# Kernel optimization log

Measured on AMD Instinct MI355X. Metric: run time of the kernel, lower is better.

## Reference

```python
import jax, jax.numpy as jnp
import numpy as np

EPS = 1e-4          # self.epsilon
STENCIL = 24        # fixed neighbor count


def _apply_G(x, coeffs, neighbors, N):
    """SpMV: y_i = G_ii * x_i + sum_j G_ij * x_{nbr[i,j]}.
    x: [B,N,1], coeffs: [B,N,25], neighbors: [B,N,24] (>=N means invalid)."""
    B = x.shape[0]
    mask = neighbors < N                                   # [B,N,24]
    safe = jnp.where(mask, neighbors, 0)
    x2 = x[..., 0]                                         # [B,N]
    x_nbrs = jnp.take_along_axis(x2, safe.reshape(B, -1), axis=1)
    x_nbrs = x_nbrs.reshape(B, -1, STENCIL) * mask.astype(x.dtype)
    res = x2 * coeffs[:, :, 0] + (x_nbrs * coeffs[:, :, 1:]).sum(axis=2)
    return res[..., None]                                  # [B,N,1]


def _apply_GT(x, coeffs, neighbors, N):
    """Transpose SpMV (scatter-add): y_{nbr[i,j]} += G_ij * x_i."""
    B = x.shape[0]
    mask = neighbors < N
    tgt = jnp.where(mask, neighbors, 0)                    # safe targets; masked vals are 0
    vals = (x * coeffs[:, :, 1:]) * mask.astype(x.dtype)   # [B,N,24]
    res = x[..., 0] * coeffs[:, :, 0]                      # [B,N]
    res = jax.vmap(lambda r, t, v: r.at[t].add(v))(
        res, tgt.reshape(B, -1), vals.reshape(B, -1))
    return res[..., None]                                  # [B,N,1]


def setup_inputs() -> dict:
    key = jax.random.key(0)
    kG, kAd, kAo, kw, kn = jax.random.split(key, 5)
    B, N = 2, 262144
    G_coeffs = jax.random.normal(kG, (B, N, 25), dtype=jnp.float32)
    A_diag = jax.random.normal(kAd, (B, N, 1), dtype=jnp.float32)
    A_off = jax.random.normal(kAo, (B, N, STENCIL), dtype=jnp.float32)
    w = jax.random.normal(kw, (B, N, 1), dtype=jnp.float32)
    valid_mask = jnp.ones((B, N, 1), dtype=jnp.float32)
    neighbors = jax.random.randint(kn, (B, N, STENCIL), 0, 270000, dtype=jnp.int64)
    return {"G_coeffs": G_coeffs, "A_diag": A_diag, "A_off": A_off,
            "w": w, "valid_mask": valid_mask, "neighbors": neighbors}


def reference(G_coeffs, A_diag, A_off, w, valid_mask, neighbors):
    B, N, _ = G_coeffs.shape
    active = valid_mask.sum()
    norm_A = (jnp.abs(A_diag).sum() + jnp.abs(A_off).sum()) / (active * 25 + 1e-6)
    # single probe vector (num_probe_vectors = 1)
    wm = w * valid_mask                                    # probe, masked
    u = _apply_GT(wm, G_coeffs, neighbors, N)
    v = _apply_G(u, G_coeffs, neighbors, N) + EPS * wm
    A_coeffs = jnp.concatenate([A_diag, A_off], axis=2)    # [B,N,25]
    y = _apply_G(v, A_coeffs, neighbors, N)
    z = y / (norm_A + 1e-8)
    diff = (z - wm) * valid_mask
    return (diff ** 2).sum() / (valid_mask.sum() + 1e-6)
```

## Files before the change

kernel.cpp:

```cpp
#include <hip/hip_runtime.h>
#include <stdint.h>

#define STENCIL 24
#define EPS_F 1e-4f
#define BLK 256
#define NXCD 8

#define NODE_N 262144
#define BIN_NODES 2048
#define LBINS 128
#define NBINS 256
#define BIN_CAP_G 49152

#define S_THREADS 512
#define S_EPT 16
#define EDGES_PER_BLOCK (S_THREADS * S_EPT)

typedef int   i32x2 __attribute__((ext_vector_type(2)));

template <typename T>
static __device__ __forceinline__ T ntload(const T* p) {
    return __builtin_nontemporal_load(p);
}

static __device__ __forceinline__ int get_xcc_id() {
    int x;
    asm volatile("s_getreg_b32 %0, hwreg(HW_REG_XCC_ID)" : "=s"(x));
    return x & (NXCD - 1);
}

__device__ __forceinline__ float wave_reduce_f32(float v) {
    #pragma unroll
    for (int off = 32; off > 0; off >>= 1)
        v += __shfl_down(v, off, 64);
    return v;
}

__device__ __forceinline__ float block_reduce_f32(float v) {
    __shared__ float sw[BLK / 64];
    float s = wave_reduce_f32(v);
    if ((threadIdx.x & 63) == 0) sw[threadIdx.x >> 6] = s;
    __syncthreads();
    float r = 0.f;
    if (threadIdx.x == 0) {
        #pragma unroll
        for (int k = 0; k < BLK / 64; ++k) r += sw[k];
    }
    return r;
}

__global__ void k_reduce(const float* __restrict__ Ad, const float* __restrict__ Ao,
                         const float* __restrict__ mask, long long BN,
                         float* __restrict__ pn, float* __restrict__ pa) {
    long long total = BN * STENCIL;
    long long stride = (long long)gridDim.x * blockDim.x;
    float s = 0.f, act = 0.f;
    for (long long t = (long long)blockIdx.x * blockDim.x + threadIdx.x; t < total; t += stride) {
        s += fabsf(ntload(Ao + t));
        if (t < BN) { s += fabsf(ntload(Ad + t)); act += ntload(mask + t); }
    }
    float bs = block_reduce_f32(s);
    if (threadIdx.x == 0) pn[blockIdx.x] = bs;
    __syncthreads();
    float ba = block_reduce_f32(act);
    if (threadIdx.x == 0) pa[blockIdx.x] = ba;
}

__global__ void k_scal(const float* __restrict__ pn, const float* __restrict__ pa,
                       int nblk, double* __restrict__ scal) {
    float sn = 0.f, sa = 0.f;
    for (int t = threadIdx.x; t < nblk; t += blockDim.x) { sn += pn[t]; sa += pa[t]; }
    float bn_ = block_reduce_f32(sn);
    __shared__ double dn;
    if (threadIdx.x == 0) dn = (double)bn_;
    __syncthreads();
    float ba = block_reduce_f32(sa);
    if (threadIdx.x == 0) {
        double act = (double)ba;
        scal[0] = dn / (act * 25.0 + 1e-6);
        scal[1] = act;
    }
}

__global__ __launch_bounds__(S_THREADS)
void k_sortscatter(const float* __restrict__ G, const float* __restrict__ w,
                   const float* __restrict__ mask, const int* __restrict__ nbr,
                   float* __restrict__ u, int* __restrict__ binCnt,
                   int2* __restrict__ pairs) {
    __shared__ int2 rec[EDGES_PER_BLOCK];
    __shared__ int hist[LBINS], incl[LBINS], excl[LBINS], pos[LBINS], gb[LBINS];
    int tid = threadIdx.x;
    if (tid < LBINS) hist[tid] = 0;
    __syncthreads();

    long long blockStart = (long long)blockIdx.x * EDGES_PER_BLOCK;
    long long t0 = blockStart + (long long)tid * S_EPT;

    int nb[S_EPT];
    const int4* p4 = (const int4*)(nbr + t0);
    #pragma unroll
    for (int q = 0; q < S_EPT / 4; ++q) {
        int4 x = p4[q];
        nb[q*4] = x.x; nb[q*4+1] = x.y; nb[q*4+2] = x.z; nb[q*4+3] = x.w;
    }
    #pragma unroll
    for (int e = 0; e < S_EPT; ++e) {
        unsigned n = (unsigned)nb[e];
        if (n < (unsigned)NODE_N) atomicAdd(&hist[n >> 11], 1);
    }
    __syncthreads();

    if (tid < LBINS) incl[tid] = hist[tid];
    __syncthreads();
    for (int d = 1; d < LBINS; d <<= 1) {
        int x = 0;
        if (tid < LBINS && tid >= d) x = incl[tid - d];
        __syncthreads();
        if (tid < LBINS) incl[tid] += x;
        __syncthreads();
    }
    int batchBase = (blockStart >= (long long)NODE_N * STENCIL) ? LBINS : 0;
    if (tid < LBINS) {
        int h = hist[tid];
        int ex = incl[tid] - h;
        excl[tid] = ex;
        pos[tid]  = ex;
        gb[tid]   = h ? atomicAdd(&binCnt[batchBase + tid], h) : 0;
    }
    __syncthreads();

    long long i0 = t0 / STENCIL;
    long long i1 = (t0 + S_EPT - 1) / STENCIL;
    float wm0 = w[i0] * mask[i0];
    float wm1 = (i1 != i0) ? w[i1] * mask[i1] : wm0;
    long long i = i0;
    int j = (int)(t0 - i0 * STENCIL);
    #pragma unroll
    for (int e = 0; e < S_EPT; ++e) {
        float wm = (i == i0) ? wm0 : wm1;
        if (j == 0) u[i] = wm * G[i * 25];
        unsigned n = (unsigned)nb[e];
        if (n < (unsigned)NODE_N) {
            int b = (int)(n >> 11);
            float val = wm * G[i * 25 + 1 + j];
            int lp = atomicAdd(&pos[b], 1);
            rec[lp] = make_int2((int)(n & (BIN_NODES - 1)) | (b << 11), __float_as_int(val));
        }
        if (++j == STENCIL) { j = 0; ++i; }
    }
    __syncthreads();

    int tot = incl[LBINS - 1];
    for (int s = tid; s < tot; s += S_THREADS) {
        int2 r = rec[s];
        int b = (r.x >> 11) & (LBINS - 1);
        int dst = gb[b] + (s - excl[b]);
        if (dst < BIN_CAP_G)
            pairs[(long long)(batchBase + b) * BIN_CAP_G + dst] =
                make_int2(r.x & (BIN_NODES - 1), r.y);
    }
}

__global__ __launch_bounds__(1024)
void k_binaccum(const int* __restrict__ binCnt, const int2* __restrict__ pairs,
                float* __restrict__ u) {
    __shared__ float acc[4][BIN_NODES + 1];
    int g = blockIdx.x, tid = threadIdx.x;
    for (int l = tid; l < BIN_NODES; l += 1024) {
        acc[0][l] = 0.f; acc[1][l] = 0.f; acc[2][l] = 0.f; acc[3][l] = 0.f;
    }
    __syncthreads();
    int cnt = binCnt[g]; if (cnt > BIN_CAP_G) cnt = BIN_CAP_G;
    const i32x2* pb = (const i32x2*)(pairs + (long long)g * BIN_CAP_G);
    int rep = tid & 3;
    for (int s = tid; s < cnt; s += 1024) {
        i32x2 r = __builtin_nontemporal_load(pb + s);
        atomicAdd(&acc[rep][r.x], __int_as_float(r.y));
    }
    __syncthreads();
    long long gbase = (long long)(g >> 7) * NODE_N + (long long)(g & (LBINS - 1)) * BIN_NODES;
    for (int l = tid; l < BIN_NODES; l += 1024)
        u[gbase + l] += acc[0][l] + acc[1][l] + acc[2][l] + acc[3][l];
}

__global__ __launch_bounds__(BLK)
void k_v(const float* __restrict__ G, const float* __restrict__ w,
         const float* __restrict__ mask, const int* __restrict__ nbr,
         const float* __restrict__ u, float* __restrict__ v, long long BN) {
    __shared__ float sg[BLK * 25];
    __shared__ int  snb[BLK * 25];
    int tid = threadIdx.x;
    long long base = (long long)blockIdx.x * BLK;
    int rows = (int)(((BN - base) < BLK) ? (BN - base) : BLK);
    const float* gsrc = G + base * 25;
    for (int k = tid; k < rows * 25; k += BLK) sg[k] = ntload(gsrc + k);
    const int* nsrc = nbr + base * STENCIL;
    for (int k = tid; k < rows * STENCIL; k += BLK) {
        int r = k / STENCIL, c = k - r * STENCIL;
        snb[r * 25 + c] = ntload(nsrc + k);
    }
    __syncthreads();
    if (tid >= rows) return;
    long long i = base + tid;
    const float* g  = sg + tid * 25;
    const int*   nn = snb + tid * 25;
    const float* ub = u + (i / NODE_N) * (long long)NODE_N;
    float acc = u[i] * g[0] + EPS_F * ntload(w + i) * ntload(mask + i);
    #pragma unroll
    for (int j = 0; j < STENCIL; ++j) {
        int n = nn[j];
        if ((unsigned)n < (unsigned)NODE_N) acc += g[1 + j] * ub[n];
    }
    v[i] = acc;
}

__global__ __launch_bounds__(BLK)
void k_y(const float* __restrict__ Ad, const float* __restrict__ Ao,
         const float* __restrict__ w, const float* __restrict__ mask,
         const int* __restrict__ nbr, const float* __restrict__ v,
         const double* __restrict__ scal, float* __restrict__ py, long long BN) {
    __shared__ float sa[BLK * 25];
    __shared__ int  snb[BLK * 25];
    int tid = threadIdx.x;
    long long base = (long long)blockIdx.x * BLK;
    int rows = (int)(((BN - base) < BLK) ? (BN - base) : BLK);
    const float* asrc = Ao + base * STENCIL;
    const int*   nsrc = nbr + base * STENCIL;
    for (int k = tid; k < rows * STENCIL; k += BLK) {
        int r = k / STENCIL, c = k - r * STENCIL;
        sa[r * 25 + c]  = ntload(asrc + k);
        snb[r * 25 + c] = ntload(nsrc + k);
    }
    __syncthreads();
    float dsq = 0.f;
    if (tid < rows) {
        long long i = base + tid;
        const float* a  = sa + tid * 25;
        const int*   nn = snb + tid * 25;
        const float* vb = v + (i / NODE_N) * (long long)NODE_N;
        float acc = v[i] * ntload(Ad + i);
        #pragma unroll
        for (int j = 0; j < STENCIL; ++j) {
            int n = nn[j];
            if ((unsigned)n < (unsigned)NODE_N) acc += a[j] * vb[n];
        }
        float z = acc / (float)(scal[0] + 1e-8);
        float m = ntload(mask + i);
        float d = (z - ntload(w + i) * m) * m;
        dsq = d * d;
    }
    float bs = block_reduce_f32(dsq);
    if (threadIdx.x == 0) py[blockIdx.x] = bs;
}

__global__ void k_final(const float* __restrict__ py, int nblk,
                        const double* __restrict__ scal, float* __restrict__ out) {
    float s = 0.f;
    for (int t = threadIdx.x; t < nblk; t += blockDim.x) s += py[t];
    float bs = block_reduce_f32(s);
    if (threadIdx.x == 0) out[0] = (float)((double)bs / (scal[1] + 1e-6));
}

__global__ void k_init_fb(const float* __restrict__ G, const float* __restrict__ w,
                          const float* __restrict__ mask, float* __restrict__ u, long long BN) {
    long long i = (long long)blockIdx.x * blockDim.x + threadIdx.x;
    if (i < BN) u[i] = w[i] * mask[i] * G[i * 25];
}
__global__ void k_scatter_fb(const float* __restrict__ G, const float* __restrict__ w,
                             const float* __restrict__ mask, const int* __restrict__ nbr,
                             float* __restrict__ ucopy, int N, long long BN) {
    long long t = (long long)blockIdx.x * blockDim.x + threadIdx.x;
    if (t >= BN * STENCIL) return;
    long long i = t / STENCIL;
    int j = (int)(t - i * STENCIL);
    int n = nbr[t];
    if ((unsigned)n >= (unsigned)N) return;
    float wm = w[i] * mask[i];
    float gv = G[i * 25 + 1 + j];
    float* ub = ucopy + (long long)get_xcc_id() * BN + (i / N) * (long long)N;
    __hip_atomic_fetch_add(&ub[n], wm * gv, __ATOMIC_RELAXED, __HIP_MEMORY_SCOPE_WORKGROUP);
}
__global__ void k_usum_fb(const float* __restrict__ ucopy, float* __restrict__ u, long long BN) {
    long long i = (long long)blockIdx.x * blockDim.x + threadIdx.x;
    if (i >= BN) return;
    float acc = u[i];
    #pragma unroll
    for (int c = 0; c < NXCD; ++c) acc += ucopy[(long long)c * BN + i];
    u[i] = acc;
}

extern "C" void kernel_launch(void* const* d_in, const int* in_sizes, int n_in,
                              void* d_out, int out_size, void* d_ws, size_t ws_size,
                              hipStream_t stream) {
    const float* G    = (const float*)d_in[0];
    const float* Ad   = (const float*)d_in[1];
    const float* Ao   = (const float*)d_in[2];
    const float* w    = (const float*)d_in[3];
    const float* mask = (const float*)d_in[4];
    const int*   nbr  = (const int*)d_in[5];

    const long long BN = in_sizes[3];
    const long long nEdges = BN * STENCIL;
    const int nodeBlocks = (int)((BN + BLK - 1) / BLK);

    float* u  = (float*)d_ws;
    float* v  = u + BN;
    float* pn = v + BN;
    float* pa = pn + 1024;
    float* py = pa + 1024;
    char*  after_common = (char*)(py + nodeBlocks);

    int*  binCnt = (int*)(((uintptr_t)after_common + 15) & ~(uintptr_t)15);
    int2* pairs  = (int2*)(((uintptr_t)(binCnt + NBINS) + 7) & ~(uintptr_t)7);
    double* scal_fast = (double*)(((uintptr_t)(pairs + (long long)NBINS * BIN_CAP_G) + 7) & ~(uintptr_t)7);
    size_t need_fast = (size_t)((char*)(scal_fast + 2) - (char*)d_ws);

    float* ucopy = (float*)(((uintptr_t)after_common + 15) & ~(uintptr_t)15);
    double* scal_fb = (double*)(((uintptr_t)(ucopy + (long long)NXCD * BN) + 7) & ~(uintptr_t)7);

    bool fast = (BN == 2LL * NODE_N) && (ws_size >= need_fast);

    k_reduce<<<1024, BLK, 0, stream>>>(Ad, Ao, mask, BN, pn, pa);

    if (fast) {
        double* scal = scal_fast;
        k_scal<<<1, BLK, 0, stream>>>(pn, pa, 1024, scal);
        hipMemsetAsync(binCnt, 0, NBINS * sizeof(int), stream);
        int gridS = (int)(nEdges / EDGES_PER_BLOCK);
        k_sortscatter<<<gridS, S_THREADS, 0, stream>>>(G, w, mask, nbr, u, binCnt, pairs);
        k_binaccum<<<NBINS, 1024, 0, stream>>>(binCnt, pairs, u);
        k_v<<<(int)(BN / BLK), BLK, 0, stream>>>(G, w, mask, nbr, u, v, BN);
        k_y<<<nodeBlocks, BLK, 0, stream>>>(Ad, Ao, w, mask, nbr, v, scal, py, BN);
        k_final<<<1, BLK, 0, stream>>>(py, nodeBlocks, scal, (float*)d_out);
    } else {
        double* scal = scal_fb;
        k_scal<<<1, BLK, 0, stream>>>(pn, pa, 1024, scal);
        hipMemsetAsync(ucopy, 0, (size_t)NXCD * BN * sizeof(float), stream);
        int edgeBlocks = (int)((nEdges + BLK - 1) / BLK);
        k_init_fb<<<nodeBlocks, BLK, 0, stream>>>(G, w, mask, u, BN);
        k_scatter_fb<<<edgeBlocks, BLK, 0, stream>>>(G, w, mask, nbr, ucopy, NODE_N, BN);
        k_usum_fb<<<nodeBlocks, BLK, 0, stream>>>(ucopy, u, BN);
        k_v<<<nodeBlocks, BLK, 0, stream>>>(G, w, mask, nbr, u, v, BN);
        k_y<<<nodeBlocks, BLK, 0, stream>>>(Ad, Ao, w, mask, nbr, v, scal, py, BN);
        k_final<<<1, BLK, 0, stream>>>(py, nodeBlocks, scal, (float*)d_out);
    }
}
```

Measured before the change: 478.4 us.

## Fuse norm reduction into k_y via expanded-square loss, drop separate reduce kernels

Removes the standalone k_reduce/k_scal pass over A_off, A_diag and mask. The |A| sums and the active count are instead accumulated inside k_y, which already streams those arrays. The loss is rebuilt algebraically in k_final from sums of P², PQ and Q², so the norm is no longer needed before k_y. Neighbor indices in k_v/k_y are now loaded straight into registers as int4 instead of being staged through shared memory, and the sortscatter edges-per-thread is halved. The expanded-square formula risks cancellation error in float accumulation.

```diff
diff --git a/kernel.cpp b/kernel.cpp
--- a/kernel.cpp
+++ b/kernel.cpp
@@ -13,7 +13,7 @@
 #define BIN_CAP_G 49152
 
 #define S_THREADS 512
-#define S_EPT 16
+#define S_EPT 8
 #define EDGES_PER_BLOCK (S_THREADS * S_EPT)
 
 typedef int   i32x2 __attribute__((ext_vector_type(2)));
@@ -36,49 +36,19 @@
     return v;
 }
 
-__device__ __forceinline__ float block_reduce_f32(float v) {
-    __shared__ float sw[BLK / 64];
-    float s = wave_reduce_f32(v);
-    if ((threadIdx.x & 63) == 0) sw[threadIdx.x >> 6] = s;
-    __syncthreads();
-    float r = 0.f;
+__device__ __forceinline__ void block_reduce5(float v[5], float out[5]) {
+    __shared__ float sw[4][5];
+    #pragma unroll
+    for (int c = 0; c < 5; ++c) v[c] = wave_reduce_f32(v[c]);
+    if ((threadIdx.x & 63) == 0) {
+        #pragma unroll
+        for (int c = 0; c < 5; ++c) sw[threadIdx.x >> 6][c] = v[c];
+    }
+    __syncthreads();
     if (threadIdx.x == 0) {
         #pragma unroll
-        for (int k = 0; k < BLK / 64; ++k) r += sw[k];
-    }
-    return r;
-}
-
-__global__ void k_reduce(const float* __restrict__ Ad, const float* __restrict__ Ao,
-                         const float* __restrict__ mask, long long BN,
-                         float* __restrict__ pn, float* __restrict__ pa) {
-    long long total = BN * STENCIL;
-    long long stride = (long long)gridDim.x * blockDim.x;
-    float s = 0.f, act = 0.f;
-    for (long long t = (long long)blockIdx.x * blockDim.x + threadIdx.x; t < total; t += stride) {
-        s += fabsf(ntload(Ao + t));
-        if (t < BN) { s += fabsf(ntload(Ad + t)); act += ntload(mask + t); }
-    }
-    float bs = block_reduce_f32(s);
-    if (threadIdx.x == 0) pn[blockIdx.x] = bs;
-    __syncthreads();
-    float ba = block_reduce_f32(act);
-    if (threadIdx.x == 0) pa[blockIdx.x] = ba;
-}
-
-__global__ void k_scal(const float* __restrict__ pn, const float* __restrict__ pa,
-                       int nblk, double* __restrict__ scal) {
-    float sn = 0.f, sa = 0.f;
-    for (int t = threadIdx.x; t < nblk; t += blockDim.x) { sn += pn[t]; sa += pa[t]; }
-    float bn_ = block_reduce_f32(sn);
-    __shared__ double dn;
-    if (threadIdx.x == 0) dn = (double)bn_;
-    __syncthreads();
-    float ba = block_reduce_f32(sa);
-    if (threadIdx.x == 0) {
-        double act = (double)ba;
-        scal[0] = dn / (act * 25.0 + 1e-6);
-        scal[1] = act;
+        for (int c = 0; c < 5; ++c)
+            out[c] = sw[0][c] + sw[1][c] + sw[2][c] + sw[3][c];
     }
 }
 
@@ -188,22 +158,22 @@
          const float* __restrict__ mask, const int* __restrict__ nbr,
          const float* __restrict__ u, float* __restrict__ v, long long BN) {
     __shared__ float sg[BLK * 25];
-    __shared__ int  snb[BLK * 25];
     int tid = threadIdx.x;
     long long base = (long long)blockIdx.x * BLK;
     int rows = (int)(((BN - base) < BLK) ? (BN - base) : BLK);
     const float* gsrc = G + base * 25;
     for (int k = tid; k < rows * 25; k += BLK) sg[k] = ntload(gsrc + k);
-    const int* nsrc = nbr + base * STENCIL;
-    for (int k = tid; k < rows * STENCIL; k += BLK) {
-        int r = k / STENCIL, c = k - r * STENCIL;
-        snb[r * 25 + c] = ntload(nsrc + k);
-    }
     __syncthreads();
     if (tid >= rows) return;
     long long i = base + tid;
+    const int4* nb4 = (const int4*)(nbr + i * STENCIL);
+    int nn[24];
+    #pragma unroll
+    for (int q = 0; q < 6; ++q) {
+        int4 x = nb4[q];
+        nn[q*4] = x.x; nn[q*4+1] = x.y; nn[q*4+2] = x.z; nn[q*4+3] = x.w;
+    }
     const float* g  = sg + tid * 25;
-    const int*   nn = snb + tid * 25;
     const float* ub = u + (i / NODE_N) * (long long)NODE_N;
     float acc = u[i] * g[0] + EPS_F * ntload(w + i) * ntload(mask + i);
     #pragma unroll
@@ -218,47 +188,85 @@
 void k_y(const float* __restrict__ Ad, const float* __restrict__ Ao,
          const float* __restrict__ w, const float* __restrict__ mask,
          const int* __restrict__ nbr, const float* __restrict__ v,
-         const double* __restrict__ scal, float* __restrict__ py, long long BN) {
+         float* __restrict__ py, int nblk, long long BN) {
     __shared__ float sa[BLK * 25];
-    __shared__ int  snb[BLK * 25];
     int tid = threadIdx.x;
     long long base = (long long)blockIdx.x * BLK;
     int rows = (int)(((BN - base) < BLK) ? (BN - base) : BLK);
     const float* asrc = Ao + base * STENCIL;
-    const int*   nsrc = nbr + base * STENCIL;
+    float asum = 0.f;
     for (int k = tid; k < rows * STENCIL; k += BLK) {
+        float x = ntload(asrc + k);
+        asum += fabsf(x);
         int r = k / STENCIL, c = k - r * STENCIL;
-        sa[r * 25 + c]  = ntload(asrc + k);
-        snb[r * 25 + c] = ntload(nsrc + k);
-    }
-    __syncthreads();
-    float dsq = 0.f;
+        sa[r * 25 + c] = x;
+    }
+    __syncthreads();
+    float part[5] = {asum, 0.f, 0.f, 0.f, 0.f};
     if (tid < rows) {
         long long i = base + tid;
+        const int4* nb4 = (const int4*)(nbr + i * STENCIL);
+        int nn[24];
+        #pragma unroll
+        for (int q = 0; q < 6; ++q) {
+            int4 x = nb4[q];
+            nn[q*4] = x.x; nn[q*4+1] = x.y; nn[q*4+2] = x.z; nn[q*4+3] = x.w;
+        }
+        float ad = ntload(Ad + i);
+        part[0] += fabsf(ad);
         const float* a  = sa + tid * 25;
-        const int*   nn = snb + tid * 25;
         const float* vb = v + (i / NODE_N) * (long long)NODE_N;
-        float acc = v[i] * ntload(Ad + i);
+        float acc = v[i] * ad;
         #pragma unroll
         for (int j = 0; j < STENCIL; ++j) {
             int n = nn[j];
             if ((unsigned)n < (unsigned)NODE_N) acc += a[j] * vb[n];
         }
-        float z = acc / (float)(scal[0] + 1e-8);
         float m = ntload(mask + i);
-        float d = (z - ntload(w + i) * m) * m;
-        dsq = d * d;
-    }
-    float bs = block_reduce_f32(dsq);
-    if (threadIdx.x == 0) py[blockIdx.x] = bs;
-}
-
-__global__ void k_final(const float* __restrict__ py, int nblk,
-                        const double* __restrict__ scal, float* __restrict__ out) {
-    float s = 0.f;
-    for (int t = threadIdx.x; t < nblk; t += blockDim.x) s += py[t];
-    float bs = block_reduce_f32(s);
-    if (threadIdx.x == 0) out[0] = (float)((double)bs / (scal[1] + 1e-6));
+        float P = acc * m;
+        float Q = ntload(w + i) * m * m;
+        part[1] = m;
+        part[2] = P * P;
+        part[3] = P * Q;
+        part[4] = Q * Q;
+    }
+    float out[5];
+    block_reduce5(part, out);
+    if (tid == 0) {
+        #pragma unroll
+        for (int c = 0; c < 5; ++c) py[(long long)c * nblk + blockIdx.x] = out[c];
+    }
+}
+
+__global__ __launch_bounds__(1024)
+void k_final(const float* __restrict__ py, int nblk, float* __restrict__ out) {
+    __shared__ float sw[16][5];
+    __shared__ float res[5];
+    float part[5] = {0.f, 0.f, 0.f, 0.f, 0.f};
+    for (int t = threadIdx.x; t < nblk; t += 1024) {
+        #pragma unroll
+        for (int c = 0; c < 5; ++c) part[c] += py[(long long)c * nblk + t];
+    }
+    #pragma unroll
+    for (int c = 0; c < 5; ++c) part[c] = wave_reduce_f32(part[c]);
+    if ((threadIdx.x & 63) == 0) {
+        #pragma unroll
+        for (int c = 0; c < 5; ++c) sw[threadIdx.x >> 6][c] = part[c];
+    }
+    __syncthreads();
+    if (threadIdx.x == 0) {
+        #pragma unroll
+        for (int c = 0; c < 5; ++c) {
+            float r = 0.f;
+            for (int k = 0; k < 16; ++k) r += sw[k][c];
+            res[c] = r;
+        }
+        double A   = res[0], act = res[1];
+        double a   = res[2], b   = res[3], c2 = res[4];
+        double nrm = A / (act * 25.0 + 1e-6) + 1e-8;
+        double loss = (a / (nrm * nrm) - 2.0 * b / nrm + c2) / (act + 1e-6);
+        out[0] = (float)loss;
+    }
 }
 
 __global__ void k_init_fb(const float* __restrict__ G, const float* __restrict__ w,
@@ -305,43 +313,31 @@
 
     float* u  = (float*)d_ws;
     float* v  = u + BN;
-    float* pn = v + BN;
-    float* pa = pn + 1024;
-    float* py = pa + 1024;
-    char*  after_common = (char*)(py + nodeBlocks);
+    float* py = v + BN;
+    char*  after_common = (char*)(py + 5LL * nodeBlocks);
 
     int*  binCnt = (int*)(((uintptr_t)after_common + 15) & ~(uintptr_t)15);
     int2* pairs  = (int2*)(((uintptr_t)(binCnt + NBINS) + 7) & ~(uintptr_t)7);
-    double* scal_fast = (double*)(((uintptr_t)(pairs + (long long)NBINS * BIN_CAP_G) + 7) & ~(uintptr_t)7);
-    size_t need_fast = (size_t)((char*)(scal_fast + 2) - (char*)d_ws);
+    size_t need_fast = (size_t)((char*)(pairs + (long long)NBINS * BIN_CAP_G) - (char*)d_ws);
 
     float* ucopy = (float*)(((uintptr_t)after_common + 15) & ~(uintptr_t)15);
-    double* scal_fb = (double*)(((uintptr_t)(ucopy + (long long)NXCD * BN) + 7) & ~(uintptr_t)7);
-
-    bool fast = (BN == 2LL * NODE_N) && (ws_size >= need_fast);
-
-    k_reduce<<<1024, BLK, 0, stream>>>(Ad, Ao, mask, BN, pn, pa);
+
+    bool fast = (BN == 2LL * NODE_N) && (nEdges % EDGES_PER_BLOCK == 0) &&
+                (ws_size >= need_fast);
 
     if (fast) {
-        double* scal = scal_fast;
-        k_scal<<<1, BLK, 0, stream>>>(pn, pa, 1024, scal);
         hipMemsetAsync(binCnt, 0, NBINS * sizeof(int), stream);
         int gridS = (int)(nEdges / EDGES_PER_BLOCK);
         k_sortscatter<<<gridS, S_THREADS, 0, stream>>>(G, w, mask, nbr, u, binCnt, pairs);
         k_binaccum<<<NBINS, 1024, 0, stream>>>(binCnt, pairs, u);
-        k_v<<<(int)(BN / BLK), BLK, 0, stream>>>(G, w, mask, nbr, u, v, BN);
-        k_y<<<nodeBlocks, BLK, 0, stream>>>(Ad, Ao, w, mask, nbr, v, scal, py, BN);
-        k_final<<<1, BLK, 0, stream>>>(py, nodeBlocks, scal, (float*)d_out);
     } else {
-        double* scal = scal_fb;
-        k_scal<<<1, BLK, 0, stream>>>(pn, pa, 1024, scal);
         hipMemsetAsync(ucopy, 0, (size_t)NXCD * BN * sizeof(float), stream);
         int edgeBlocks = (int)((nEdges + BLK - 1) / BLK);
         k_init_fb<<<nodeBlocks, BLK, 0, stream>>>(G, w, mask, u, BN);
         k_scatter_fb<<<edgeBlocks, BLK, 0, stream>>>(G, w, mask, nbr, ucopy, NODE_N, BN);
         k_usum_fb<<<nodeBlocks, BLK, 0, stream>>>(ucopy, u, BN);
-        k_v<<<nodeBlocks, BLK, 0, stream>>>(G, w, mask, nbr, u, v, BN);
-        k_y<<<nodeBlocks, BLK, 0, stream>>>(Ad, Ao, w, mask, nbr, v, scal, py, BN);
-        k_final<<<1, BLK, 0, stream>>>(py, nodeBlocks, scal, (float*)d_out);
-    }
-}
+    }
+    k_v<<<nodeBlocks, BLK, 0, stream>>>(G, w, mask, nbr, u, v, BN);
+    k_y<<<nodeBlocks, BLK, 0, stream>>>(Ad, Ao, w, mask, nbr, v, py, nodeBlocks, BN);
+    k_final<<<1, 1024, 0, stream>>>(py, nodeBlocks, (float*)d_out);
+}
```

New measurement: 407.4 us. 1.17x faster.
